# Performance work log

Hardware: AMD Instinct MI355X
Metric: run time of the kernel (lower is better)

## Reference

```python
import jax, jax.numpy as jnp
import numpy as np

COST_CLASS, COST_MASK, COST_DICE = 1.0, 1.0, 1.0
ALPHA, GAMMA = 0.25, 2.0


def setup_inputs() -> dict:
    key = jax.random.key(0)
    k1, k2, k3, k4 = jax.random.split(key, 4)
    B, Q, C, H, W, T, Hm, Wm = 2, 100, 134, 256, 256, 20, 512, 512
    return {
        "masks_queries_logits": jax.random.normal(k1, (B, Q, H, W), jnp.float32),
        "class_queries_logits": jax.random.normal(k2, (B, Q, C), jnp.float32),
        "mask_labels": jax.random.uniform(k3, (B, T, Hm, Wm), dtype=jnp.float32),
        "class_labels": jax.random.randint(k4, (B, T), 0, C),
    }


def _nearest_resize(x, H, W):
    # torch F.interpolate(mode='nearest'): src_idx = floor(dst_idx * in / out)
    Hi, Wi = x.shape[-2], x.shape[-1]
    ri = (jnp.arange(H) * Hi) // H
    ci = (jnp.arange(W) * Wi) // W
    return x[..., ri, :][..., ci]


def _cost_matrices(masks_queries_logits, class_queries_logits, mask_labels, class_labels):
    B, Q, H, W = masks_queries_logits.shape
    HW = H * W
    tgt = _nearest_resize(mask_labels, H, W)                       # [B,T,H,W]
    probs = jax.nn.softmax(class_queries_logits, axis=-1)          # [B,Q,C]
    # cost_class = -probs[:, labels]  -> [B,Q,T]
    cost_class = -jnp.take_along_axis(
        probs, jnp.broadcast_to(class_labels[:, None, :], (B, Q, class_labels.shape[1])), axis=2
    )
    x = masks_queries_logits.reshape(B, Q, HW)                     # [B,Q,HW]
    lab = tgt.reshape(B, -1, HW)                                   # [B,T,HW]
    p = jax.nn.sigmoid(x)
    ce_pos = jax.nn.softplus(-x)   # BCEWithLogits(target=1)
    ce_neg = jax.nn.softplus(x)    # BCEWithLogits(target=0)
    focal_pos = ALPHA * (1.0 - p) ** GAMMA * ce_pos
    focal_neg = (1.0 - ALPHA) * p ** GAMMA * ce_neg
    cost_mask = (jnp.einsum('bqk,btk->bqt', focal_pos, lab)
                 + jnp.einsum('bqk,btk->bqt', focal_neg, 1.0 - lab)) / HW
    numer = 2.0 * jnp.einsum('bqk,btk->bqt', p, lab)
    denom = p.sum(-1)[:, :, None] + lab.sum(-1)[:, None, :]
    cost_dice = 1.0 - (numer + 1.0) / (denom + 1.0)
    return COST_MASK * cost_mask + COST_CLASS * cost_class + COST_DICE * cost_dice


def _hungarian(cost):
    # Exact O(n^3) Hungarian (Jonker-Volgenant style potentials), numpy on host.
    # Zero-pads to square like the torch code; dummy cols all-zero so the real
    # assignment equals the rectangular optimum.
    n_rows, n_cols = cost.shape
    n = max(n_rows, n_cols)
    a = np.zeros((n + 1, n + 1), dtype=np.float64)
    a[1:n_rows + 1, 1:n_cols + 1] = cost
    u = np.zeros(n + 1); v = np.zeros(n + 1)
    p = np.zeros(n + 1, dtype=np.int64)
    way = np.zeros(n + 1, dtype=np.int64)
    for i in range(1, n + 1):
        p[0] = i; j0 = 0
        minv = np.full(n + 1, np.inf)
        used = np.zeros(n + 1, dtype=bool)
        while True:
            used[j0] = True
            i0 = p[j0]
            cur = a[i0, 1:] - u[i0] - v[1:]
            free = ~used[1:]
            upd = free & (cur < minv[1:])
            minv[1:][upd] = cur[upd]
            way[1:][upd] = j0
            cand = np.where(free, minv[1:], np.inf)
            j1 = int(np.argmin(cand)) + 1
            delta = cand[j1 - 1]
            u[p[used]] += delta
            v[used] -= delta
            minv[1:][free] -= delta
            j0 = j1
            if p[j0] == 0:
                break
        while j0:
            j1 = way[j0]
            p[j0] = p[j1]
            j0 = j1
    rows, cols = [], []
    for j in range(1, n_cols + 1):
        r = p[j] - 1
        if 0 <= r < n_rows:
            rows.append(r); cols.append(j - 1)
    rows = np.asarray(rows, dtype=np.int64)
    cols = np.asarray(cols, dtype=np.int64)
    order = np.argsort(rows)  # torch impl emits pairs in ascending row order
    return rows[order], cols[order]


def reference(masks_queries_logits, class_queries_logits, mask_labels, class_labels):
    cost = _cost_matrices(masks_queries_logits, class_queries_logits, mask_labels, class_labels)
    cost_np = np.asarray(jax.device_get(cost), dtype=np.float64)  # [B,Q,T]
    pairs = [np.stack(_hungarian(c)) for c in cost_np]            # each [2, min(Q,T)]
    return jnp.asarray(np.stack(pairs), dtype=jnp.int32)          # [B, 2, T]
```

## Files before the change

kernel.cpp:

```cpp
#include <hip/hip_runtime.h>
#include <hip/hip_bf16.h>
#include <math.h>

#define HW_   65536
#define B_    2
#define Q_    100
#define C_    134
#define T_    20
#define NHUN  100
#define MT_   7
#define KSB   128
#define BKCH  512
#define PREC  1088
#define CPAD  21

typedef __attribute__((ext_vector_type(8))) short bf16x8;
typedef __attribute__((ext_vector_type(4))) float f32x4;

#define LABPS_OFF  0
#define CC_OFF     512
#define COST_OFF   4608
#define BASE_END   8704
#define LABT_HI_F  BASE_END
#define PART_OFF   (LABT_HI_F + 1310720)
#define CSUM_OFF   (PART_OFF + B_ * KSB * MT_ * PREC)
#define WS_END_F   (CSUM_OFF + B_ * MT_ * 1056)

__device__ inline unsigned short f2bf(float f) {
    unsigned int u = __builtin_bit_cast(unsigned int, f);
    u += 0x7FFFu + ((u >> 16) & 1u);
    return (unsigned short)(u >> 16);
}
__device__ inline float softplusf(float x) {
    float ax = fabsf(x);
    return fmaxf(x, 0.0f) + log1pf(expf(-ax));
}

__global__ void lab_prep_kernel(const float* __restrict__ ml, unsigned short* __restrict__ labT,
                                float* __restrict__ lab_ps, int writeT) {
    int b = blockIdx.x, t = blockIdx.y, ksl = blockIdx.z;
    int tid = threadIdx.x;
    const float* src = ml + (size_t)(b * T_ + t) * 262144;
    size_t dst = ((size_t)(b * T_ + t)) << 16;
    float acc = 0.f;
    for (int it = 0; it < 8; ++it) {
        int k = ksl * 8192 + it * 1024 + tid * 4;
        int r = k >> 8, c = k & 255;
        const float* s = src + r * 1024 + 2 * c;
        float4 u = *(const float4*)s;
        float4 w = *(const float4*)(s + 4);
        float v[4] = {u.x, u.z, w.x, w.z};
        unsigned short h[4];
#pragma unroll
        for (int e = 0; e < 4; ++e) { h[e] = f2bf(v[e]); acc += v[e]; }
        if (writeT) *(ushort4*)(labT + dst + k) = make_ushort4(h[0], h[1], h[2], h[3]);
    }
    for (int off = 32; off > 0; off >>= 1) acc += __shfl_down(acc, off);
    __shared__ float sb[4];
    int wid = tid >> 6, lane = tid & 63;
    if (lane == 0) sb[wid] = acc;
    __syncthreads();
    if (tid == 0) lab_ps[(b * T_ + t) * 8 + ksl] = sb[0] + sb[1] + sb[2] + sb[3];
}

__global__ void class_cost_kernel(const float* __restrict__ cl, const int* __restrict__ labels,
                                  float* __restrict__ cc) {
    int bq  = blockIdx.x;
    int b   = bq / Q_;
    int tid = threadIdx.x;
    __shared__ float sl[C_];
    const float* src = cl + (size_t)bq * C_;
    for (int c = tid; c < C_; c += 64) sl[c] = src[c];
    __syncthreads();
    float mx = -INFINITY;
    for (int c = tid; c < C_; c += 64) mx = fmaxf(mx, sl[c]);
    for (int off = 32; off > 0; off >>= 1) mx = fmaxf(mx, __shfl_xor(mx, off));
    float se = 0.f;
    for (int c = tid; c < C_; c += 64) se += expf(sl[c] - mx);
    for (int off = 32; off > 0; off >>= 1) se += __shfl_xor(se, off);
    float inv = 1.0f / se;
    if (tid < T_) {
        int lbl = labels[b * T_ + tid];
        cc[bq * T_ + tid] = -expf(sl[lbl] - mx) * inv;
    }
}

__global__ __launch_bounds__(256) void focal_mfma_kernel(
        const float* __restrict__ mq, const unsigned short* __restrict__ labT,
        float* __restrict__ part) {
    int idx = blockIdx.x;
    int mt  = idx % MT_;
    int rem = idx / MT_;
    int ks  = rem % KSB;
    int b   = rem / KSB;
    int tid  = threadIdx.x;
    int wave = tid >> 6, lane = tid & 63;
    int lg = lane >> 4, lr = lane & 15;

    int q = mt * 16 + lr;
    bool qok = (q < Q_);
    const float* xrow = mq + ((size_t)(b * Q_ + (qok ? q : 0)) << 16);
    int koff = ks * BKCH + wave * 128 + lg * 8;

    const unsigned short* b1 = labT + (((size_t)(b * T_ + lr)) << 16);
    const unsigned short* b2 = labT + (((size_t)(b * T_ + 16 + (lr & 3))) << 16);
    bool n2row = (lr < 4);

    f32x4 accD0 = {0,0,0,0}, accD1 = {0,0,0,0};
    f32x4 accP0 = {0,0,0,0}, accP1 = {0,0,0,0};
    float F = 0.f, P = 0.f;

    bf16x8 zer;
#pragma unroll
    for (int e = 0; e < 8; ++e) zer[e] = 0;

    for (int kk = 0; kk < 4; ++kk) {
        int kb = koff + kk * 32;
        float4 u0 = *(const float4*)(xrow + kb);
        float4 u1 = *(const float4*)(xrow + kb + 4);
        float xv[8] = {u0.x, u0.y, u0.z, u0.w, u1.x, u1.y, u1.z, u1.w};

        bf16x8 f1 = *(const bf16x8*)(b1 + kb);
        bf16x8 f2 = n2row ? *(const bf16x8*)(b2 + kb) : zer;

        bf16x8 dh, ph;
#pragma unroll
        for (int e = 0; e < 8; ++e) {
            float x  = xv[e];
            float ax = fabsf(x);
            float a  = __expf(-ax);
            float rr = 1.0f / (1.0f + a);
            float p  = (x >= 0.f) ? rr : a * rr;
            float om = (x >= 0.f) ? a * rr : rr;
            float l1 = __logf(1.0f + a);
            float spn = fmaxf(-x, 0.f) + l1;
            float spp = spn + x;
            float fp = 0.25f * om * om * spn;
            float fn = 0.75f * p * p * spp;
            F += fn; P += p;
            dh[e] = (short)f2bf(fp - fn);
            ph[e] = (short)f2bf(p);
        }
        accD0 = __builtin_amdgcn_mfma_f32_16x16x32_bf16(dh, f1, accD0, 0, 0, 0);
        accD1 = __builtin_amdgcn_mfma_f32_16x16x32_bf16(dh, f2, accD1, 0, 0, 0);
        accP0 = __builtin_amdgcn_mfma_f32_16x16x32_bf16(ph, f1, accP0, 0, 0, 0);
        accP1 = __builtin_amdgcn_mfma_f32_16x16x32_bf16(ph, f2, accP1, 0, 0, 0);
    }

    F += __shfl_down(F, 32); F += __shfl_down(F, 16);
    P += __shfl_down(P, 32); P += __shfl_down(P, 16);

    __shared__ float red[4][4][64][4];
    __shared__ float fpb[4][2][16];
#pragma unroll
    for (int r = 0; r < 4; ++r) {
        red[wave][0][lane][r] = accD0[r];
        red[wave][1][lane][r] = accD1[r];
        red[wave][2][lane][r] = accP0[r];
        red[wave][3][lane][r] = accP1[r];
    }
    if (lane < 16) { fpb[wave][0][lane] = F; fpb[wave][1][lane] = P; }
    __syncthreads();
    for (int e = tid; e < 1024; e += 256) {
        int f  = e >> 8;
        int l2 = (e & 255) >> 2;
        int r  = e & 3;
        part[(size_t)idx * PREC + e] =
            red[0][f][l2][r] + red[1][f][l2][r] + red[2][f][l2][r] + red[3][f][l2][r];
    }
    if (tid < 16)
        part[(size_t)idx * PREC + 1024 + tid] =
            fpb[0][0][tid] + fpb[1][0][tid] + fpb[2][0][tid] + fpb[3][0][tid];
    else if (tid < 32) {
        int l = tid - 16;
        part[(size_t)idx * PREC + 1040 + l] =
            fpb[0][1][l] + fpb[1][1][l] + fpb[2][1][l] + fpb[3][1][l];
    }
}

__global__ __launch_bounds__(256) void reduce_part_kernel(const float* __restrict__ part,
                                                          float* __restrict__ Csum) {
    int bm   = blockIdx.x;
    int mt   = bm % MT_;
    int b    = bm / MT_;
    int tid  = threadIdx.x;
    int epos = tid & 31;
    int grp  = tid >> 5;
    int e    = blockIdx.y * 32 + epos;

    const float* base = part + (size_t)((b * KSB) * MT_ + mt) * PREC + e;
    float s = 0.f;
    for (int k = 0; k < 16; ++k) {
        s += base[(size_t)(grp * 16 + k) * MT_ * PREC];
    }
    __shared__ float red[8][33];
    red[grp][epos] = s;
    __syncthreads();
    if (tid < 32) {
        float tot = 0.f;
        for (int g = 0; g < 8; ++g) tot += red[g][tid];
        Csum[(size_t)bm * 1056 + e] = tot;
    }
}

__global__ __launch_bounds__(320) void compose_kernel(
        const float* __restrict__ Csum, const float* __restrict__ cl,
        const int* __restrict__ labels, const float* __restrict__ lab_ps,
        float* __restrict__ cost) {
    int bm = blockIdx.x;
    int mt = bm % MT_;
    int b  = bm / MT_;
    int tid = threadIdx.x;
    int q0 = mt * 16;

    __shared__ float sl[16][136];
    __shared__ float mx[16], se[16];
    __shared__ int   lbl[T_];
    for (int e = tid; e < 16 * C_; e += 320) {
        int qm = e / C_, c = e % C_;
        int q = q0 + qm;
        sl[qm][c] = (q < Q_) ? cl[(size_t)(b * Q_ + q) * C_ + c] : 0.f;
    }
    if (tid < T_) lbl[tid] = labels[b * T_ + tid];
    __syncthreads();
    if (tid < 16) {
        float m = -INFINITY;
        for (int c = 0; c < C_; ++c) m = fmaxf(m, sl[tid][c]);
        float s = 0.f;
        for (int c = 0; c < C_; ++c) s += expf(sl[tid][c] - m);
        mx[tid] = m; se[tid] = s;
    }
    __syncthreads();

    int qm = tid / T_, t = tid % T_;
    int q = q0 + qm;
    if (qm < 16 && q < Q_) {
        const float* C = Csum + (size_t)bm * 1056;
        int nt   = t >> 4;
        int lane = ((qm >> 2) << 4) | (t & 15);
        int reg  = qm & 3;
        float Sd = C[(0 + nt) * 256 + lane * 4 + reg];
        float Sp = C[(2 + nt) * 256 + lane * 4 + reg];
        float F  = C[1024 + qm];
        float P  = C[1040 + qm];
        float L = 0.f;
        for (int s8 = 0; s8 < 8; ++s8) L += lab_ps[(b * T_ + t) * 8 + s8];
        float ccv = -expf(sl[qm][lbl[t]] - mx[qm]) / se[qm];
        float cm = (Sd + F) * (1.0f / (float)HW_);
        float cd = 1.0f - (2.0f * Sp + 1.0f) / (P + L + 1.0f);
        cost[(size_t)(b * Q_ + q) * T_ + t] = cm + cd + ccv;
    }
}

__global__ __launch_bounds__(1024) void mask_cost_mono_kernel(
        const float* __restrict__ mq, const float* __restrict__ ml,
        const float* __restrict__ cc, const float* __restrict__ lab_ps,
        float* __restrict__ cost) {
    int bq  = blockIdx.x;
    int b   = bq / Q_;
    int tid = threadIdx.x;
    const float* xb  = mq + (size_t)bq * HW_;
    const float* mlb = ml + (size_t)b * T_ * 262144;
    float s1[T_], s2[T_];
#pragma unroll
    for (int t = 0; t < T_; ++t) { s1[t] = 0.f; s2[t] = 0.f; }
    float F = 0.f, P = 0.f;
    for (int k = tid; k < HW_; k += 1024) {
        int i = k >> 8, j = k & 255;
        float x = xb[k];
        float p = 1.0f / (1.0f + expf(-x));
        float spn = softplusf(-x);
        float spp = softplusf(x);
        float om = 1.0f - p;
        float fp = 0.25f * om * om * spn;
        float fn = 0.75f * p * p * spp;
        F += fn; P += p;
        float diff = fp - fn;
        int off0 = i * 1024 + 2 * j;
#pragma unroll
        for (int t = 0; t < T_; ++t) {
            float lab = mlb[t * 262144 + off0];
            s1[t] = fmaf(diff, lab, s1[t]);
            s2[t] = fmaf(p,    lab, s2[t]);
        }
    }
    __shared__ float sbuf[16][42];
    int wid = tid >> 6, lane = tid & 63;
#pragma unroll
    for (int t = 0; t < T_; ++t) {
        for (int off = 32; off > 0; off >>= 1) {
            s1[t] += __shfl_down(s1[t], off);
            s2[t] += __shfl_down(s2[t], off);
        }
    }
    for (int off = 32; off > 0; off >>= 1) { F += __shfl_down(F, off); P += __shfl_down(P, off); }
    if (lane == 0) {
#pragma unroll
        for (int t = 0; t < T_; ++t) { sbuf[wid][t] = s1[t]; sbuf[wid][T_ + t] = s2[t]; }
        sbuf[wid][40] = F; sbuf[wid][41] = P;
    }
    __syncthreads();
    if (tid < T_) {
        float S1 = 0.f, S2 = 0.f, Fs = 0.f, Ps = 0.f;
        for (int w = 0; w < 16; ++w) {
            S1 += sbuf[w][tid]; S2 += sbuf[w][T_ + tid];
            Fs += sbuf[w][40];  Ps += sbuf[w][41];
        }
        float L = 0.f;
        for (int sl = 0; sl < 8; ++sl) L += lab_ps[(b * T_ + tid) * 8 + sl];
        float cm = (S1 + Fs) * (1.0f / (float)HW_);
        float cd = 1.0f - (2.0f * S2 + 1.0f) / (Ps + L + 1.0f);
        cost[bq * T_ + tid] = cm + cd + cc[bq * T_ + tid];
    }
}

__global__ __launch_bounds__(64) void hungarian_kernel(const float* __restrict__ cost,
                                                       int* __restrict__ out) {
    int b    = blockIdx.x;
    int lane = threadIdx.x;

    __shared__ float csh[Q_ * CPAD];
    __shared__ int   psh[NHUN + 1];

    for (int j = lane; j < Q_; j += 64) {
#pragma unroll
        for (int t = 0; t < T_; ++t)
            csh[j * CPAD + t] = cost[b * Q_ * T_ + j * T_ + t];
    }
    __syncthreads();

    const int ja = lane;
    const int jb = lane + 64;
    const bool ja_ok = (ja >= 1);
    const bool jb_ok = (jb <= NHUN);

    int   p_a = 0, p_b = 0;
    float v_a = 0.f, v_b = 0.f;
    float u_reg = 0.f;

    for (int i = 1; i <= T_; ++i) {
        float ca = ja_ok ? csh[(ja - 1) * CPAD + (i - 1)] : INFINITY;
        float cb = jb_ok ? csh[(jb - 1) * CPAD + (i - 1)] : INFINITY;
        float vmin = fminf(ca, cb);
        for (int off = 32; off > 0; off >>= 1)
            vmin = fminf(vmin, __shfl_xor(vmin, off));
        unsigned long long ba = __ballot(ca == vmin);
        int j1 = ba ? (__ffsll(ba) - 1) : (__ffsll(__ballot(cb == vmin)) - 1 + 64);
        if (lane == i) u_reg = vmin;
        int pj = __shfl((j1 < 64) ? p_a : p_b, j1 & 63);
        if (pj == 0) {
            if (j1 < 64) { if (lane == j1) p_a = i; }
            else         { if (lane == j1 - 64) p_b = i; }
        }
    }

    for (int i = 1; i <= T_; ++i) {
        bool mine = (p_a == i) || (p_b == i);
        if (__ballot(mine)) continue;

        float m_a = INFINITY, m_b = INFINITY;
        int   way_a = 0, way_b = 0;
        bool  us_a = false, us_b = false;
        bool  in_tree = (lane == i);
        int   j0 = 0, jf;

        while (true) {
            int i0 = (j0 == 0) ? i : __shfl((j0 < 64) ? p_a : p_b, j0 & 63);
            if (lane == i0) in_tree = true;
            float ui0 = __shfl(u_reg, i0);
            if (ja == j0) us_a = true;
            if (jb == j0) us_b = true;
            bool fa = ja_ok && !us_a;
            bool fb = jb_ok && !us_b;
            if (fa) {
                float cur = csh[(ja - 1) * CPAD + (i0 - 1)] - ui0 - v_a;
                if (cur < m_a) { m_a = cur; way_a = j0; }
            }
            if (fb) {
                float cur = csh[(jb - 1) * CPAD + (i0 - 1)] - ui0 - v_b;
                if (cur < m_b) { m_b = cur; way_b = j0; }
            }
            float ca = fa ? m_a : INFINITY;
            float cb = fb ? m_b : INFINITY;
            float vmin = fminf(ca, cb);
            for (int off = 32; off > 0; off >>= 1)
                vmin = fminf(vmin, __shfl_xor(vmin, off));
            unsigned long long ba = __ballot(ca == vmin);
            int j1 = ba ? (__ffsll(ba) - 1) : (__ffsll(__ballot(cb == vmin)) - 1 + 64);
            float delta = vmin;
            if (us_a) v_a -= delta; else m_a -= delta;
            if (us_b) v_b -= delta; else m_b -= delta;
            if (in_tree) u_reg += delta;
            j0 = j1;
            int pj0 = __shfl((j0 < 64) ? p_a : p_b, j0 & 63);
            if (pj0 == 0) { jf = j0; break; }
        }
        int jj = jf;
        while (jj) {
            int wv = __shfl((jj < 64) ? way_a : way_b, jj & 63);
            int pn = (wv == 0) ? i : __shfl((wv < 64) ? p_a : p_b, wv & 63);
            if (jj < 64) { if (lane == jj) p_a = pn; }
            else         { if (lane == jj - 64) p_b = pn; }
            jj = wv;
        }
    }

    if (ja_ok) psh[ja] = p_a;
    if (jb_ok) psh[jb] = p_b;
    if (lane == 0) psh[0] = 0;
    __syncthreads();
    if (lane == 0) {
        int* ob = out + b * 2 * T_;
        int k = 0;
        for (int j = 1; j <= NHUN; ++j) {
            if (psh[j] != 0) { ob[k] = j - 1; ob[T_ + k] = psh[j] - 1; ++k; }
        }
    }
}

extern "C" void kernel_launch(void* const* d_in, const int* in_sizes, int n_in,
                              void* d_out, int out_size, void* d_ws, size_t ws_size,
                              hipStream_t stream) {
    const float* mq     = (const float*)d_in[0];
    const float* cl     = (const float*)d_in[1];
    const float* ml     = (const float*)d_in[2];
    const int*   labels = (const int*)d_in[3];
    int* out = (int*)d_out;
    float* ws = (float*)d_ws;

    float* lab_ps = ws + LABPS_OFF;
    float* cc     = ws + CC_OFF;
    float* cost   = ws + COST_OFF;

    size_t need = (size_t)WS_END_F * 4;

    if (ws_size >= need) {
        unsigned short* labT = (unsigned short*)(ws + LABT_HI_F);
        float* part = ws + PART_OFF;
        float* Csum = ws + CSUM_OFF;
        hipLaunchKernelGGL(lab_prep_kernel,   dim3(B_, T_, 8), dim3(256), 0, stream,
                           ml, labT, lab_ps, 1);
        hipLaunchKernelGGL(focal_mfma_kernel, dim3(B_ * KSB * MT_), dim3(256), 0, stream,
                           mq, labT, part);
        hipLaunchKernelGGL(reduce_part_kernel, dim3(B_ * MT_, 33), dim3(256), 0, stream,
                           part, Csum);
        hipLaunchKernelGGL(compose_kernel,    dim3(B_ * MT_),  dim3(320), 0, stream,
                           Csum, cl, labels, lab_ps, cost);
    } else {
        hipLaunchKernelGGL(lab_prep_kernel,   dim3(B_, T_, 8), dim3(256), 0, stream,
                           ml, (unsigned short*)ws, lab_ps, 0);
        hipLaunchKernelGGL(class_cost_kernel, dim3(B_ * Q_),   dim3(64),  0, stream, cl, labels, cc);
        hipLaunchKernelGGL(mask_cost_mono_kernel, dim3(B_ * Q_), dim3(1024), 0, stream,
                           mq, ml, cc, lab_ps, cost);
    }
    hipLaunchKernelGGL(hungarian_kernel, dim3(B_), dim3(64), 0, stream, cost, out);
}
```

Baseline: 70.89 us.

## Fuse label resize/convert into focal MFMA and compose into Hungarian kernel

Drops the separate lab_prep pass that wrote a bf16 transposed label buffer. The focal MFMA kernel now reads the strided fp32 mask labels directly and converts them to bf16 in registers. Label sums come from a spare ones-row in the last query tile, and the cost composition (softmax class cost plus dice and focal terms) moves into the Hungarian kernel's prologue, so two launches and one intermediate round-trip go away. The costs are heavier strided global reads in the hot MFMA kernel (only half of each fetched sector is used) and a serial per-query softmax inside a 2-block kernel.

```diff
diff --git a/kernel.cpp b/kernel.cpp
--- a/kernel.cpp
+++ b/kernel.cpp
@@ -21,8 +21,7 @@
 #define CC_OFF     512
 #define COST_OFF   4608
 #define BASE_END   8704
-#define LABT_HI_F  BASE_END
-#define PART_OFF   (LABT_HI_F + 1310720)
+#define PART_OFF   BASE_END
 #define CSUM_OFF   (PART_OFF + B_ * KSB * MT_ * PREC)
 #define WS_END_F   (CSUM_OFF + B_ * MT_ * 1056)
 
@@ -36,57 +35,8 @@
     return fmaxf(x, 0.0f) + log1pf(expf(-ax));
 }
 
-__global__ void lab_prep_kernel(const float* __restrict__ ml, unsigned short* __restrict__ labT,
-                                float* __restrict__ lab_ps, int writeT) {
-    int b = blockIdx.x, t = blockIdx.y, ksl = blockIdx.z;
-    int tid = threadIdx.x;
-    const float* src = ml + (size_t)(b * T_ + t) * 262144;
-    size_t dst = ((size_t)(b * T_ + t)) << 16;
-    float acc = 0.f;
-    for (int it = 0; it < 8; ++it) {
-        int k = ksl * 8192 + it * 1024 + tid * 4;
-        int r = k >> 8, c = k & 255;
-        const float* s = src + r * 1024 + 2 * c;
-        float4 u = *(const float4*)s;
-        float4 w = *(const float4*)(s + 4);
-        float v[4] = {u.x, u.z, w.x, w.z};
-        unsigned short h[4];
-#pragma unroll
-        for (int e = 0; e < 4; ++e) { h[e] = f2bf(v[e]); acc += v[e]; }
-        if (writeT) *(ushort4*)(labT + dst + k) = make_ushort4(h[0], h[1], h[2], h[3]);
-    }
-    for (int off = 32; off > 0; off >>= 1) acc += __shfl_down(acc, off);
-    __shared__ float sb[4];
-    int wid = tid >> 6, lane = tid & 63;
-    if (lane == 0) sb[wid] = acc;
-    __syncthreads();
-    if (tid == 0) lab_ps[(b * T_ + t) * 8 + ksl] = sb[0] + sb[1] + sb[2] + sb[3];
-}
-
-__global__ void class_cost_kernel(const float* __restrict__ cl, const int* __restrict__ labels,
-                                  float* __restrict__ cc) {
-    int bq  = blockIdx.x;
-    int b   = bq / Q_;
-    int tid = threadIdx.x;
-    __shared__ float sl[C_];
-    const float* src = cl + (size_t)bq * C_;
-    for (int c = tid; c < C_; c += 64) sl[c] = src[c];
-    __syncthreads();
-    float mx = -INFINITY;
-    for (int c = tid; c < C_; c += 64) mx = fmaxf(mx, sl[c]);
-    for (int off = 32; off > 0; off >>= 1) mx = fmaxf(mx, __shfl_xor(mx, off));
-    float se = 0.f;
-    for (int c = tid; c < C_; c += 64) se += expf(sl[c] - mx);
-    for (int off = 32; off > 0; off >>= 1) se += __shfl_xor(se, off);
-    float inv = 1.0f / se;
-    if (tid < T_) {
-        int lbl = labels[b * T_ + tid];
-        cc[bq * T_ + tid] = -expf(sl[lbl] - mx) * inv;
-    }
-}
-
-__global__ __launch_bounds__(256) void focal_mfma_kernel(
-        const float* __restrict__ mq, const unsigned short* __restrict__ labT,
+__global__ __launch_bounds__(256, 4) void focal_mfma_kernel(
+        const float* __restrict__ mq, const float* __restrict__ ml,
         float* __restrict__ part) {
     int idx = blockIdx.x;
     int mt  = idx % MT_;
@@ -102,27 +52,51 @@
     const float* xrow = mq + ((size_t)(b * Q_ + (qok ? q : 0)) << 16);
     int koff = ks * BKCH + wave * 128 + lg * 8;
 
-    const unsigned short* b1 = labT + (((size_t)(b * T_ + lr)) << 16);
-    const unsigned short* b2 = labT + (((size_t)(b * T_ + 16 + (lr & 3))) << 16);
-    bool n2row = (lr < 4);
+    const float* mlb1 = ml + ((size_t)(b * T_ + lr) << 18);
+    const float* mlb2 = ml + ((size_t)(b * T_ + 16 + (lr & 3)) << 18);
+    bool n2row   = (lr < 4);
+    bool onesrow = (mt == 6) && (lr == 4);
 
     f32x4 accD0 = {0,0,0,0}, accD1 = {0,0,0,0};
     f32x4 accP0 = {0,0,0,0}, accP1 = {0,0,0,0};
     float F = 0.f, P = 0.f;
 
-    bf16x8 zer;
-#pragma unroll
-    for (int e = 0; e < 8; ++e) zer[e] = 0;
-
+    bf16x8 zer, one;
+#pragma unroll
+    for (int e = 0; e < 8; ++e) { zer[e] = 0; one[e] = (short)0x3F80; }
+
+#pragma unroll
     for (int kk = 0; kk < 4; ++kk) {
         int kb = koff + kk * 32;
+        int r  = kb >> 8, c = kb & 255;
+        int soff = r * 1024 + 2 * c;
+
         float4 u0 = *(const float4*)(xrow + kb);
         float4 u1 = *(const float4*)(xrow + kb + 4);
+        float4 s0 = *(const float4*)(mlb1 + soff);
+        float4 s1 = *(const float4*)(mlb1 + soff + 4);
+        float4 s2 = *(const float4*)(mlb1 + soff + 8);
+        float4 s3 = *(const float4*)(mlb1 + soff + 12);
+        float4 t0 = *(const float4*)(mlb2 + soff);
+        float4 t1 = *(const float4*)(mlb2 + soff + 4);
+        float4 t2 = *(const float4*)(mlb2 + soff + 8);
+        float4 t3 = *(const float4*)(mlb2 + soff + 12);
+
+        bf16x8 f1, f2;
+        f1[0] = (short)f2bf(s0.x); f1[1] = (short)f2bf(s0.z);
+        f1[2] = (short)f2bf(s1.x); f1[3] = (short)f2bf(s1.z);
+        f1[4] = (short)f2bf(s2.x); f1[5] = (short)f2bf(s2.z);
+        f1[6] = (short)f2bf(s3.x); f1[7] = (short)f2bf(s3.z);
+        if (n2row) {
+            f2[0] = (short)f2bf(t0.x); f2[1] = (short)f2bf(t0.z);
+            f2[2] = (short)f2bf(t1.x); f2[3] = (short)f2bf(t1.z);
+            f2[4] = (short)f2bf(t2.x); f2[5] = (short)f2bf(t2.z);
+            f2[6] = (short)f2bf(t3.x); f2[7] = (short)f2bf(t3.z);
+        } else {
+            f2 = zer;
+        }
+
         float xv[8] = {u0.x, u0.y, u0.z, u0.w, u1.x, u1.y, u1.z, u1.w};
-
-        bf16x8 f1 = *(const bf16x8*)(b1 + kb);
-        bf16x8 f2 = n2row ? *(const bf16x8*)(b2 + kb) : zer;
-
         bf16x8 dh, ph;
 #pragma unroll
         for (int e = 0; e < 8; ++e) {
@@ -141,6 +115,8 @@
             dh[e] = (short)f2bf(fp - fn);
             ph[e] = (short)f2bf(p);
         }
+        if (onesrow) { dh = one; ph = one; }
+
         accD0 = __builtin_amdgcn_mfma_f32_16x16x32_bf16(dh, f1, accD0, 0, 0, 0);
         accD1 = __builtin_amdgcn_mfma_f32_16x16x32_bf16(dh, f2, accD1, 0, 0, 0);
         accP0 = __builtin_amdgcn_mfma_f32_16x16x32_bf16(ph, f1, accP0, 0, 0, 0);
@@ -161,12 +137,16 @@
     }
     if (lane < 16) { fpb[wave][0][lane] = F; fpb[wave][1][lane] = P; }
     __syncthreads();
-    for (int e = tid; e < 1024; e += 256) {
-        int f  = e >> 8;
-        int l2 = (e & 255) >> 2;
-        int r  = e & 3;
-        part[(size_t)idx * PREC + e] =
-            red[0][f][l2][r] + red[1][f][l2][r] + red[2][f][l2][r] + red[3][f][l2][r];
+    {
+        int e4 = tid;
+        int f  = e4 >> 6;
+        int l2 = e4 & 63;
+        float4 s;
+        s.x = red[0][f][l2][0] + red[1][f][l2][0] + red[2][f][l2][0] + red[3][f][l2][0];
+        s.y = red[0][f][l2][1] + red[1][f][l2][1] + red[2][f][l2][1] + red[3][f][l2][1];
+        s.z = red[0][f][l2][2] + red[1][f][l2][2] + red[2][f][l2][2] + red[3][f][l2][2];
+        s.w = red[0][f][l2][3] + red[1][f][l2][3] + red[2][f][l2][3] + red[3][f][l2][3];
+        *(float4*)(part + (size_t)idx * PREC + e4 * 4) = s;
     }
     if (tid < 16)
         part[(size_t)idx * PREC + 1024 + tid] =
@@ -190,9 +170,8 @@
 
     const float* base = part + (size_t)((b * KSB) * MT_ + mt) * PREC + e;
     float s = 0.f;
-    for (int k = 0; k < 16; ++k) {
+    for (int k = 0; k < 16; ++k)
         s += base[(size_t)(grp * 16 + k) * MT_ * PREC];
-    }
     __shared__ float red[8][33];
     red[grp][epos] = s;
     __syncthreads();
@@ -203,52 +182,190 @@
     }
 }
 
-__global__ __launch_bounds__(320) void compose_kernel(
+__global__ __launch_bounds__(256) void hungarian_kernel(
         const float* __restrict__ Csum, const float* __restrict__ cl,
-        const int* __restrict__ labels, const float* __restrict__ lab_ps,
-        float* __restrict__ cost) {
-    int bm = blockIdx.x;
-    int mt = bm % MT_;
-    int b  = bm / MT_;
+        const int* __restrict__ labels_g, const float* __restrict__ cost_g,
+        int* __restrict__ out, int fused) {
+    int b   = blockIdx.x;
     int tid = threadIdx.x;
-    int q0 = mt * 16;
-
-    __shared__ float sl[16][136];
-    __shared__ float mx[16], se[16];
+
+    __shared__ float csh[Q_ * CPAD];
+    __shared__ int   psh[NHUN + 1];
+    __shared__ float Lt[T_];
     __shared__ int   lbl[T_];
-    for (int e = tid; e < 16 * C_; e += 320) {
-        int qm = e / C_, c = e % C_;
-        int q = q0 + qm;
-        sl[qm][c] = (q < Q_) ? cl[(size_t)(b * Q_ + q) * C_ + c] : 0.f;
-    }
-    if (tid < T_) lbl[tid] = labels[b * T_ + tid];
-    __syncthreads();
-    if (tid < 16) {
-        float m = -INFINITY;
-        for (int c = 0; c < C_; ++c) m = fmaxf(m, sl[tid][c]);
-        float s = 0.f;
-        for (int c = 0; c < C_; ++c) s += expf(sl[tid][c] - m);
-        mx[tid] = m; se[tid] = s;
-    }
-    __syncthreads();
-
-    int qm = tid / T_, t = tid % T_;
-    int q = q0 + qm;
-    if (qm < 16 && q < Q_) {
-        const float* C = Csum + (size_t)bm * 1056;
-        int nt   = t >> 4;
-        int lane = ((qm >> 2) << 4) | (t & 15);
-        int reg  = qm & 3;
-        float Sd = C[(0 + nt) * 256 + lane * 4 + reg];
-        float Sp = C[(2 + nt) * 256 + lane * 4 + reg];
-        float F  = C[1024 + qm];
-        float P  = C[1040 + qm];
-        float L = 0.f;
-        for (int s8 = 0; s8 < 8; ++s8) L += lab_ps[(b * T_ + t) * 8 + s8];
-        float ccv = -expf(sl[qm][lbl[t]] - mx[qm]) / se[qm];
-        float cm = (Sd + F) * (1.0f / (float)HW_);
-        float cd = 1.0f - (2.0f * Sp + 1.0f) / (P + L + 1.0f);
-        cost[(size_t)(b * Q_ + q) * T_ + t] = cm + cd + ccv;
+
+    if (fused) {
+        if (tid < T_) {
+            lbl[tid] = labels_g[b * T_ + tid];
+            const float* CL = Csum + (size_t)(b * MT_ + 6) * 1056;
+            int nt = tid >> 4;
+            int ln = 16 + (tid & 15);
+            Lt[tid] = CL[(2 + nt) * 256 + ln * 4];
+        }
+        __syncthreads();
+        if (tid < Q_) {
+            int q = tid, mt = q >> 4, qm = q & 15;
+            const float* C   = Csum + (size_t)(b * MT_ + mt) * 1056;
+            const float* row = cl + (size_t)(b * Q_ + q) * C_;
+            float m = -INFINITY;
+            for (int c = 0; c < C_; ++c) m = fmaxf(m, row[c]);
+            float s = 0.f;
+            for (int c = 0; c < C_; ++c) s += expf(row[c] - m);
+            float F = C[1024 + qm];
+            float P = C[1040 + qm];
+#pragma unroll
+            for (int t = 0; t < T_; ++t) {
+                int nt = t >> 4;
+                int ln = ((qm >> 2) << 4) | (t & 15);
+                int rg = qm & 3;
+                float Sd = C[(0 + nt) * 256 + ln * 4 + rg];
+                float Sp = C[(2 + nt) * 256 + ln * 4 + rg];
+                float ccv = -expf(row[lbl[t]] - m) / s;
+                float cm = (Sd + F) * (1.0f / (float)HW_);
+                float cd = 1.0f - (2.0f * Sp + 1.0f) / (P + Lt[t] + 1.0f);
+                csh[q * CPAD + t] = cm + cd + ccv;
+            }
+        }
+    } else {
+        for (int idx = tid; idx < Q_ * T_; idx += 256) {
+            int q = idx / T_, t = idx % T_;
+            csh[q * CPAD + t] = cost_g[b * Q_ * T_ + idx];
+        }
+    }
+    __syncthreads();
+
+    if (tid < 64) {
+        int lane = tid;
+        const int ja = lane;
+        const int jb = lane + 64;
+        const bool ja_ok = (ja >= 1);
+        const bool jb_ok = (jb <= NHUN);
+
+        int   p_a = 0, p_b = 0;
+        float v_a = 0.f, v_b = 0.f;
+        float u_reg = 0.f;
+
+        for (int i = 1; i <= T_; ++i) {
+            float ca = ja_ok ? csh[(ja - 1) * CPAD + (i - 1)] : INFINITY;
+            float cb = jb_ok ? csh[(jb - 1) * CPAD + (i - 1)] : INFINITY;
+            float vmin = fminf(ca, cb);
+            for (int off = 32; off > 0; off >>= 1)
+                vmin = fminf(vmin, __shfl_xor(vmin, off));
+            unsigned long long ba = __ballot(ca == vmin);
+            int j1 = ba ? (__ffsll(ba) - 1) : (__ffsll(__ballot(cb == vmin)) - 1 + 64);
+            if (lane == i) u_reg = vmin;
+            int pj = __shfl((j1 < 64) ? p_a : p_b, j1 & 63);
+            if (pj == 0) {
+                if (j1 < 64) { if (lane == j1) p_a = i; }
+                else         { if (lane == j1 - 64) p_b = i; }
+            }
+        }
+
+        for (int i = 1; i <= T_; ++i) {
+            bool mine = (p_a == i) || (p_b == i);
+            if (__ballot(mine)) continue;
+
+            float m_a = INFINITY, m_b = INFINITY;
+            int   way_a = 0, way_b = 0;
+            bool  us_a = false, us_b = false;
+            bool  in_tree = (lane == i);
+            int   j0 = 0, jf;
+
+            while (true) {
+                int i0 = (j0 == 0) ? i : __shfl((j0 < 64) ? p_a : p_b, j0 & 63);
+                if (lane == i0) in_tree = true;
+                float ui0 = __shfl(u_reg, i0);
+                if (ja == j0) us_a = true;
+                if (jb == j0) us_b = true;
+                bool fa = ja_ok && !us_a;
+                bool fb = jb_ok && !us_b;
+                if (fa) {
+                    float cur = csh[(ja - 1) * CPAD + (i0 - 1)] - ui0 - v_a;
+                    if (cur < m_a) { m_a = cur; way_a = j0; }
+                }
+                if (fb) {
+                    float cur = csh[(jb - 1) * CPAD + (i0 - 1)] - ui0 - v_b;
+                    if (cur < m_b) { m_b = cur; way_b = j0; }
+                }
+                float ca = fa ? m_a : INFINITY;
+                float cb = fb ? m_b : INFINITY;
+                float vmin = fminf(ca, cb);
+                for (int off = 32; off > 0; off >>= 1)
+                    vmin = fminf(vmin, __shfl_xor(vmin, off));
+                unsigned long long ba = __ballot(ca == vmin);
+                int j1 = ba ? (__ffsll(ba) - 1) : (__ffsll(__ballot(cb == vmin)) - 1 + 64);
+                float delta = vmin;
+                if (us_a) v_a -= delta; else m_a -= delta;
+                if (us_b) v_b -= delta; else m_b -= delta;
+                if (in_tree) u_reg += delta;
+                j0 = j1;
+                int pj0 = __shfl((j0 < 64) ? p_a : p_b, j0 & 63);
+                if (pj0 == 0) { jf = j0; break; }
+            }
+            int jj = jf;
+            while (jj) {
+                int wv = __shfl((jj < 64) ? way_a : way_b, jj & 63);
+                int pn = (wv == 0) ? i : __shfl((wv < 64) ? p_a : p_b, wv & 63);
+                if (jj < 64) { if (lane == jj) p_a = pn; }
+                else         { if (lane == jj - 64) p_b = pn; }
+                jj = wv;
+            }
+        }
+
+        if (ja_ok) psh[ja] = p_a;
+        if (jb_ok) psh[jb] = p_b;
+        if (lane == 0) psh[0] = 0;
+    }
+    __syncthreads();
+    if (tid == 0) {
+        int* ob = out + b * 2 * T_;
+        int k = 0;
+        for (int j = 1; j <= NHUN; ++j) {
+            if (psh[j] != 0) { ob[k] = j - 1; ob[T_ + k] = psh[j] - 1; ++k; }
+        }
+    }
+}
+
+__global__ void lab_prep_kernel(const float* __restrict__ ml, float* __restrict__ lab_ps) {
+    int b = blockIdx.x, t = blockIdx.y, ksl = blockIdx.z;
+    int tid = threadIdx.x;
+    const float* src = ml + (size_t)(b * T_ + t) * 262144;
+    float acc = 0.f;
+    for (int it = 0; it < 8; ++it) {
+        int k = ksl * 8192 + it * 1024 + tid * 4;
+        int r = k >> 8, c = k & 255;
+        const float* s = src + r * 1024 + 2 * c;
+        float4 u = *(const float4*)s;
+        float4 w = *(const float4*)(s + 4);
+        acc += u.x + u.z + w.x + w.z;
+    }
+    for (int off = 32; off > 0; off >>= 1) acc += __shfl_down(acc, off);
+    __shared__ float sb[4];
+    int wid = tid >> 6, lane = tid & 63;
+    if (lane == 0) sb[wid] = acc;
+    __syncthreads();
+    if (tid == 0) lab_ps[(b * T_ + t) * 8 + ksl] = sb[0] + sb[1] + sb[2] + sb[3];
+}
+
+__global__ void class_cost_kernel(const float* __restrict__ cl, const int* __restrict__ labels,
+                                  float* __restrict__ cc) {
+    int bq  = blockIdx.x;
+    int b   = bq / Q_;
+    int tid = threadIdx.x;
+    __shared__ float sl[C_];
+    const float* src = cl + (size_t)bq * C_;
+    for (int c = tid; c < C_; c += 64) sl[c] = src[c];
+    __syncthreads();
+    float mx = -INFINITY;
+    for (int c = tid; c < C_; c += 64) mx = fmaxf(mx, sl[c]);
+    for (int off = 32; off > 0; off >>= 1) mx = fmaxf(mx, __shfl_xor(mx, off));
+    float se = 0.f;
+    for (int c = tid; c < C_; c += 64) se += expf(sl[c] - mx);
+    for (int off = 32; off > 0; off >>= 1) se += __shfl_xor(se, off);
+    float inv = 1.0f / se;
+    if (tid < T_) {
+        int lbl = labels[b * T_ + tid];
+        cc[bq * T_ + tid] = -expf(sl[lbl] - mx) * inv;
     }
 }
 
@@ -314,110 +431,6 @@
     }
 }
 
-__global__ __launch_bounds__(64) void hungarian_kernel(const float* __restrict__ cost,
-                                                       int* __restrict__ out) {
-    int b    = blockIdx.x;
-    int lane = threadIdx.x;
-
-    __shared__ float csh[Q_ * CPAD];
-    __shared__ int   psh[NHUN + 1];
-
-    for (int j = lane; j < Q_; j += 64) {
-#pragma unroll
-        for (int t = 0; t < T_; ++t)
-            csh[j * CPAD + t] = cost[b * Q_ * T_ + j * T_ + t];
-    }
-    __syncthreads();
-
-    const int ja = lane;
-    const int jb = lane + 64;
-    const bool ja_ok = (ja >= 1);
-    const bool jb_ok = (jb <= NHUN);
-
-    int   p_a = 0, p_b = 0;
-    float v_a = 0.f, v_b = 0.f;
-    float u_reg = 0.f;
-
-    for (int i = 1; i <= T_; ++i) {
-        float ca = ja_ok ? csh[(ja - 1) * CPAD + (i - 1)] : INFINITY;
-        float cb = jb_ok ? csh[(jb - 1) * CPAD + (i - 1)] : INFINITY;
-        float vmin = fminf(ca, cb);
-        for (int off = 32; off > 0; off >>= 1)
-            vmin = fminf(vmin, __shfl_xor(vmin, off));
-        unsigned long long ba = __ballot(ca == vmin);
-        int j1 = ba ? (__ffsll(ba) - 1) : (__ffsll(__ballot(cb == vmin)) - 1 + 64);
-        if (lane == i) u_reg = vmin;
-        int pj = __shfl((j1 < 64) ? p_a : p_b, j1 & 63);
-        if (pj == 0) {
-            if (j1 < 64) { if (lane == j1) p_a = i; }
-            else         { if (lane == j1 - 64) p_b = i; }
-        }
-    }
-
-    for (int i = 1; i <= T_; ++i) {
-        bool mine = (p_a == i) || (p_b == i);
-        if (__ballot(mine)) continue;
-
-        float m_a = INFINITY, m_b = INFINITY;
-        int   way_a = 0, way_b = 0;
-        bool  us_a = false, us_b = false;
-        bool  in_tree = (lane == i);
-        int   j0 = 0, jf;
-
-        while (true) {
-            int i0 = (j0 == 0) ? i : __shfl((j0 < 64) ? p_a : p_b, j0 & 63);
-            if (lane == i0) in_tree = true;
-            float ui0 = __shfl(u_reg, i0);
-            if (ja == j0) us_a = true;
-            if (jb == j0) us_b = true;
-            bool fa = ja_ok && !us_a;
-            bool fb = jb_ok && !us_b;
-            if (fa) {
-                float cur = csh[(ja - 1) * CPAD + (i0 - 1)] - ui0 - v_a;
-                if (cur < m_a) { m_a = cur; way_a = j0; }
-            }
-            if (fb) {
-                float cur = csh[(jb - 1) * CPAD + (i0 - 1)] - ui0 - v_b;
-                if (cur < m_b) { m_b = cur; way_b = j0; }
-            }
-            float ca = fa ? m_a : INFINITY;
-            float cb = fb ? m_b : INFINITY;
-            float vmin = fminf(ca, cb);
-            for (int off = 32; off > 0; off >>= 1)
-                vmin = fminf(vmin, __shfl_xor(vmin, off));
-            unsigned long long ba = __ballot(ca == vmin);
-            int j1 = ba ? (__ffsll(ba) - 1) : (__ffsll(__ballot(cb == vmin)) - 1 + 64);
-            float delta = vmin;
-            if (us_a) v_a -= delta; else m_a -= delta;
-            if (us_b) v_b -= delta; else m_b -= delta;
-            if (in_tree) u_reg += delta;
-            j0 = j1;
-            int pj0 = __shfl((j0 < 64) ? p_a : p_b, j0 & 63);
-            if (pj0 == 0) { jf = j0; break; }
-        }
-        int jj = jf;
-        while (jj) {
-            int wv = __shfl((jj < 64) ? way_a : way_b, jj & 63);
-            int pn = (wv == 0) ? i : __shfl((wv < 64) ? p_a : p_b, wv & 63);
-            if (jj < 64) { if (lane == jj) p_a = pn; }
-            else         { if (lane == jj - 64) p_b = pn; }
-            jj = wv;
-        }
-    }
-
-    if (ja_ok) psh[ja] = p_a;
-    if (jb_ok) psh[jb] = p_b;
-    if (lane == 0) psh[0] = 0;
-    __syncthreads();
-    if (lane == 0) {
-        int* ob = out + b * 2 * T_;
-        int k = 0;
-        for (int j = 1; j <= NHUN; ++j) {
-            if (psh[j] != 0) { ob[k] = j - 1; ob[T_ + k] = psh[j] - 1; ++k; }
-        }
-    }
-}
-
 extern "C" void kernel_launch(void* const* d_in, const int* in_sizes, int n_in,
                               void* d_out, int out_size, void* d_ws, size_t ws_size,
                               hipStream_t stream) {
@@ -435,23 +448,22 @@
     size_t need = (size_t)WS_END_F * 4;
 
     if (ws_size >= need) {
-        unsigned short* labT = (unsigned short*)(ws + LABT_HI_F);
         float* part = ws + PART_OFF;
         float* Csum = ws + CSUM_OFF;
-        hipLaunchKernelGGL(lab_prep_kernel,   dim3(B_, T_, 8), dim3(256), 0, stream,
-                           ml, labT, lab_ps, 1);
-        hipLaunchKernelGGL(focal_mfma_kernel, dim3(B_ * KSB * MT_), dim3(256), 0, stream,
-                           mq, labT, part);
+        hipLaunchKernelGGL(focal_mfma_kernel,  dim3(B_ * KSB * MT_), dim3(256), 0, stream,
+                           mq, ml, part);
         hipLaunchKernelGGL(reduce_part_kernel, dim3(B_ * MT_, 33), dim3(256), 0, stream,
                            part, Csum);
-        hipLaunchKernelGGL(compose_kernel,    dim3(B_ * MT_),  dim3(320), 0, stream,
-                           Csum, cl, labels, lab_ps, cost);
+        hipLaunchKernelGGL(hungarian_kernel,   dim3(B_), dim3(256), 0, stream,
+                           Csum, cl, labels, cost, out, 1);
     } else {
-        hipLaunchKernelGGL(lab_prep_kernel,   dim3(B_, T_, 8), dim3(256), 0, stream,
-                           ml, (unsigned short*)ws, lab_ps, 0);
-        hipLaunchKernelGGL(class_cost_kernel, dim3(B_ * Q_),   dim3(64),  0, stream, cl, labels, cc);
+        hipLaunchKernelGGL(lab_prep_kernel,    dim3(B_, T_, 8), dim3(256), 0, stream,
+                           ml, lab_ps);
+        hipLaunchKernelGGL(class_cost_kernel,  dim3(B_ * Q_), dim3(64), 0, stream,
+                           cl, labels, cc);
         hipLaunchKernelGGL(mask_cost_mono_kernel, dim3(B_ * Q_), dim3(1024), 0, stream,
                            mq, ml, cc, lab_ps, cost);
-    }
-    hipLaunchKernelGGL(hungarian_kernel, dim3(B_), dim3(64), 0, stream, cost, out);
-}
+        hipLaunchKernelGGL(hungarian_kernel,   dim3(B_), dim3(256), 0, stream,
+                           ws, cl, labels, cost, out, 0);
+    }
+}
```

Measured after the change: 107.9 us. 52.2% more time.
